# Kernel tuning notes

Measured on AMD Instinct MI355X. Metric: run time of the kernel, lower is better.

## Reference

```python
import jax, jax.numpy as jnp
import numpy as np


def setup_inputs() -> dict:
    key = jax.random.key(0)
    k1, k2 = jax.random.split(key)
    B, C, H, W = 8, 64, 32, 32
    K = 8192
    x = jax.random.normal(k1, (B, C, H, W), dtype=jnp.float32)
    codebook = jax.random.normal(k2, (K, C), dtype=jnp.float32)
    return {"x": x, "codebook": codebook}


def reference(x, codebook):
    """Faithful JAX version of VQVAE.quantize().

    x:        [B, C, H, W] latent (output of pre_quant_conv)
    codebook: [K, C] embedding weight
    Returns (quant_out [B,C,H,W], commitment_loss, codebook_loss, indices [B,H,W]).
    """
    B, C, H, W = x.shape
    # [B, H, W, C] -> [B, N, C]
    xf = jnp.transpose(x, (0, 2, 3, 1)).reshape(B, H * W, C)

    # Squared pairwise distances (argmin of cdist == argmin of squared dist).
    x2 = jnp.sum(xf * xf, axis=-1, keepdims=True)            # [B, N, 1]
    e2 = jnp.sum(codebook * codebook, axis=-1)               # [K]
    xe = jnp.einsum('bnc,kc->bnk', xf, codebook)             # [B, N, K]
    d2 = x2 + e2[None, None, :] - 2.0 * xe                   # [B, N, K]
    idx = jnp.argmin(d2, axis=-1)                            # [B, N]

    quant = codebook[idx.reshape(-1)]                        # [B*N, C]
    xflat = xf.reshape(-1, C)                                # [B*N, C]

    commitment_loss = jnp.mean((jax.lax.stop_gradient(quant) - xflat) ** 2)
    codebook_loss = jnp.mean((quant - jax.lax.stop_gradient(xflat)) ** 2)

    # Straight-through estimator.
    quant_st = xflat + jax.lax.stop_gradient(quant - xflat)
    quant_out = jnp.transpose(quant_st.reshape(B, H, W, C), (0, 3, 1, 2))
    indices = idx.reshape(B, H, W)
    return quant_out, commitment_loss, codebook_loss, indices
```

## Files before the change

### kernel.cpp

```cpp
#include <hip/hip_runtime.h>


#define N_PTS   8192
#define K_CODES 8192
#define C_DIM   64
#define HWSZ    1024
#define QOUT_N  524288
#define SPLITS  16

#define WS_XS    0
#define WS_CBS   2097152
#define WS_E2H   4194304
#define WS_PACK  4227072
#define WS_PART  5275648

typedef __attribute__((ext_vector_type(8))) short    short8;
typedef __attribute__((ext_vector_type(8))) _Float16 half8;
typedef __attribute__((ext_vector_type(4))) float    floatx4;

__device__ __forceinline__ half8 as_h8(short8 v) {
    return __builtin_bit_cast(half8, v);
}
__device__ __forceinline__ void split2(float v, unsigned short& h,
                                       unsigned short& m) {
    _Float16 hh = (_Float16)v;
    float r = v - (float)hh;
    _Float16 mm = (_Float16)r;
    h = __builtin_bit_cast(unsigned short, hh);
    m = __builtin_bit_cast(unsigned short, mm);
}
__device__ __forceinline__ void cp16(const void* g, void* l) {
    __builtin_amdgcn_global_load_lds(
        (const __attribute__((address_space(1))) void*)g,
        (__attribute__((address_space(3))) void*)l, 16, 0, 0);
}
__device__ __forceinline__ void cp4(const void* g, void* l) {
    __builtin_amdgcn_global_load_lds(
        (const __attribute__((address_space(1))) void*)g,
        (__attribute__((address_space(3))) void*)l, 4, 0, 0);
}

__global__ __launch_bounds__(256)
void vq_prep_kernel(const float* __restrict__ x,
                    const float* __restrict__ cb,
                    unsigned short* __restrict__ xS,
                    unsigned short* __restrict__ cbS,
                    float* __restrict__ e2h)
{
    const int bx  = blockIdx.x;
    const int tid = threadIdx.x;

    if (bx < 32) {
        const int k = bx * 256 + tid;
        const float* row = cb + k * C_DIM;
        float s = 0.0f;
        #pragma unroll
        for (int g = 0; g < 8; ++g) {
            float4 a = *(const float4*)(row + g * 8);
            float4 b = *(const float4*)(row + g * 8 + 4);
            float vv[8] = {a.x, a.y, a.z, a.w, b.x, b.y, b.z, b.w};
            unsigned short h8[8], m8[8];
            #pragma unroll
            for (int j = 0; j < 8; ++j) {
                s = fmaf(vv[j], vv[j], s);
                split2(vv[j], h8[j], m8[j]);
            }
            *(uint4*)(cbS + ((size_t)(0 * 8 + g) * 8192 + k) * 8) = *(const uint4*)h8;
            *(uint4*)(cbS + ((size_t)(1 * 8 + g) * 8192 + k) * 8) = *(const uint4*)m8;
        }
        e2h[k] = 0.5f * s;
    } else {
        const int u = bx - 32;
        const int b = u >> 5, g = (u >> 2) & 7, q = u & 3;
        const int hw = q * 256 + tid;
        const float* xb = x + (size_t)(b * C_DIM + g * 8) * HWSZ + hw;
        unsigned short h8[8], m8[8];
        #pragma unroll
        for (int cq = 0; cq < 8; ++cq)
            split2(xb[cq * HWSZ], h8[cq], m8[cq]);
        const size_t n = (size_t)b * 1024 + hw;
        *(uint4*)(xS + ((size_t)(0 * 8 + g) * 8192 + n) * 8) = *(const uint4*)h8;
        *(uint4*)(xS + ((size_t)(1 * 8 + g) * 8192 + n) * 8) = *(const uint4*)m8;
    }
}

#define SEG_SHORTS 512
#define NSEGS      16
#define BUF_SHORTS 8320

__device__ __forceinline__ void computeTile(const half8 af[4][2][2],
                                            const unsigned short* __restrict__ bsrc,
                                            int tl, int quad, int col, int code,
                                            float bestv[4][4], int besti[4][4])
{
    half8 bf[2][2];
    #pragma unroll
    for (int p = 0; p < 2; ++p)
        #pragma unroll
        for (int s = 0; s < 2; ++s) {
            int seg = p * 8 + s * 4 + quad;
            bf[p][s] = as_h8(*(const short8*)(bsrc + seg * SEG_SHORTS + (tl * 16 + col) * 8));
        }
    float me2 = -((const float*)(bsrc + NSEGS * SEG_SHORTS))[tl * 16 + col];

    floatx4 acc[4];
    #pragma unroll
    for (int t = 0; t < 4; ++t) acc[t] = (floatx4){me2, me2, me2, me2};

    #pragma unroll
    for (int s = 0; s < 2; ++s) {
        #pragma unroll
        for (int t = 0; t < 4; ++t)
            acc[t] = __builtin_amdgcn_mfma_f32_16x16x32_f16(af[t][0][s], bf[0][s], acc[t], 0, 0, 0);
        #pragma unroll
        for (int t = 0; t < 4; ++t)
            acc[t] = __builtin_amdgcn_mfma_f32_16x16x32_f16(af[t][0][s], bf[1][s], acc[t], 0, 0, 0);
        #pragma unroll
        for (int t = 0; t < 4; ++t)
            acc[t] = __builtin_amdgcn_mfma_f32_16x16x32_f16(af[t][1][s], bf[0][s], acc[t], 0, 0, 0);
    }

    #pragma unroll
    for (int t = 0; t < 4; ++t)
        #pragma unroll
        for (int r = 0; r < 4; ++r) {
            float sc = acc[t][r];
            bool gt = sc > bestv[t][r];
            bestv[t][r] = gt ? sc   : bestv[t][r];
            besti[t][r] = gt ? code : besti[t][r];
        }
}

__global__ __launch_bounds__(512, 1)
void vq_argmin_kernel(const unsigned short* __restrict__ xS,
                      const unsigned short* __restrict__ cbS,
                      const float* __restrict__ e2h,
                      unsigned long long* __restrict__ packedS)
{
    __shared__ __align__(16) unsigned short sBuf[2][BUF_SHORTS];

    const int tid   = threadIdx.x;
    const int lane  = tid & 63;
    const int w     = tid >> 6;
    const int col   = lane & 15;
    const int quad  = lane >> 4;
    const int mb    = blockIdx.x;
    const int split = blockIdx.y;
    const int m0    = mb * 512 + w * 64;
    const int nb0   = split * 512;

    half8 af[4][2][2];
    #pragma unroll
    for (int t = 0; t < 4; ++t) {
        int pt = m0 + t * 16 + col;
        #pragma unroll
        for (int p = 0; p < 2; ++p)
            #pragma unroll
            for (int s = 0; s < 2; ++s) {
                int g = s * 4 + quad;
                af[t][p][s] = as_h8(*(const short8*)(xS + ((size_t)(p * 8 + g) * 8192 + pt) * 8));
            }
    }

    float bestv[4][4];
    int   besti[4][4];
    #pragma unroll
    for (int t = 0; t < 4; ++t)
        #pragma unroll
        for (int r = 0; r < 4; ++r) {
            bestv[t][r] = __uint_as_float(0xFF800000u);
            besti[t][r] = 0;
        }

    auto stage = [&](int k0, int buf) {
        unsigned short* dst = &sBuf[buf][0];
        #pragma unroll
        for (int i = 0; i < 2; ++i) {
            int f   = tid + i * 512;
            int seg = f >> 6;
            int l   = f & 63;
            cp16(cbS + ((size_t)seg * 8192 + k0 + l) * 8,
                 dst + seg * SEG_SHORTS + l * 8);
        }
        if (tid < 64)
            cp4(e2h + k0 + tid, (float*)(dst + NSEGS * SEG_SHORTS) + tid);
    };

    stage(nb0, 0);
    __syncthreads();

    for (int ch = 0; ch < 8; ++ch) {
        if (ch + 1 < 8) stage(nb0 + (ch + 1) * 64, (ch + 1) & 1);
        const unsigned short* bsrc = &sBuf[ch & 1][0];
        #pragma unroll
        for (int tl = 0; tl < 4; ++tl)
            computeTile(af, bsrc, tl, quad, col,
                        nb0 + ch * 64 + tl * 16 + col, bestv, besti);
        __syncthreads();
    }

    unsigned long long own = 0;
    #pragma unroll
    for (int t = 0; t < 4; ++t)
        #pragma unroll
        for (int r = 0; r < 4; ++r) {
            unsigned u = __float_as_uint(-bestv[t][r]);
            u = ((int)u < 0) ? ~u : (u | 0x80000000u);
            unsigned long long p = ((unsigned long long)u << 32) | (unsigned)besti[t][r];
            #pragma unroll
            for (int msk = 1; msk < 16; msk <<= 1) {
                unsigned long long q = __shfl_xor(p, msk, 64);
                p = (q < p) ? q : p;
            }
            own = (col == t * 4 + r) ? p : own;
        }
    const int mpt = m0 + (col >> 2) * 16 + quad * 4 + (col & 3);
    packedS[(size_t)split * N_PTS + mpt] = own;
}

__global__ __launch_bounds__(256)
void vq_gather_kernel(const float* __restrict__ x,
                      const float* __restrict__ cb,
                      const unsigned long long* __restrict__ packedS,
                      float* __restrict__ out,
                      float* __restrict__ part)
{
    __shared__ unsigned long long sred[8][32];
    const int tid = threadIdx.x;
    const int p   = tid & 31;
    const int sg  = tid >> 5;
    const int n0  = blockIdx.x * 32;
    const int n   = n0 + p;

    {
        unsigned long long v = packedS[(size_t)(sg * 2) * N_PTS + n];
        unsigned long long q = packedS[(size_t)(sg * 2 + 1) * N_PTS + n];
        sred[sg][p] = (q < v) ? q : v;
    }
    __syncthreads();

    unsigned long long v = sred[0][p];
    #pragma unroll
    for (int s = 1; s < 8; ++s) {
        unsigned long long q = sred[s][p];
        v = (q < v) ? q : v;
    }
    const int idx = (int)(v & 0xFFFFFFFFull);
    if (tid < 32) out[QOUT_N + 2 + n0 + tid] = (float)idx;

    const int c0  = sg * 8;
    const int b   = n >> 10;
    const int hw  = n & 1023;
    const float* xb = x   + (size_t)b * (C_DIM * HWSZ) + hw;
    float*       ob = out + (size_t)b * (C_DIM * HWSZ) + hw;

    float s = 0.0f;
    #pragma unroll
    for (int c4 = 0; c4 < 2; ++c4) {
        float4 q = *(const float4*)(cb + (size_t)idx * C_DIM + c0 + c4 * 4);
        float qa[4] = {q.x, q.y, q.z, q.w};
        #pragma unroll
        for (int j = 0; j < 4; ++j) {
            int c = c0 + c4 * 4 + j;
            float xv = xb[c * HWSZ];
            float d  = qa[j] - xv;
            s = fmaf(d, d, s);
            ob[c * HWSZ] = xv + d;
        }
    }

    #pragma unroll
    for (int off = 32; off > 0; off >>= 1) s += __shfl_down(s, off, 64);
    if ((tid & 63) == 0) part[blockIdx.x * 4 + (tid >> 6)] = s;
}

__global__ __launch_bounds__(256)
void vq_final_kernel(const float* __restrict__ part, float* __restrict__ out)
{
    __shared__ float w[4];
    float s = part[threadIdx.x] + part[threadIdx.x + 256]
            + part[threadIdx.x + 512] + part[threadIdx.x + 768];
    #pragma unroll
    for (int off = 32; off > 0; off >>= 1) s += __shfl_down(s, off, 64);
    if ((threadIdx.x & 63) == 0) w[threadIdx.x >> 6] = s;
    __syncthreads();
    if (threadIdx.x == 0) {
        float m = (w[0] + w[1] + w[2] + w[3]) * (1.0f / (float)QOUT_N);
        out[QOUT_N]     = m;
        out[QOUT_N + 1] = m;
    }
}

extern "C" void kernel_launch(void* const* d_in, const int* in_sizes, int n_in,
                              void* d_out, int out_size, void* d_ws, size_t ws_size,
                              hipStream_t stream)
{
    const float* x  = (const float*)d_in[0];
    const float* cb = (const float*)d_in[1];
    float* out = (float*)d_out;
    char*  ws  = (char*)d_ws;
    (void)ws_size;

    unsigned short* xS  = (unsigned short*)(ws + WS_XS);
    unsigned short* cbS = (unsigned short*)(ws + WS_CBS);
    float* e2h = (float*)(ws + WS_E2H);
    unsigned long long* packedS = (unsigned long long*)(ws + WS_PACK);
    float* part = (float*)(ws + WS_PART);

    vq_prep_kernel<<<288, 256, 0, stream>>>(x, cb, xS, cbS, e2h);
    vq_argmin_kernel<<<dim3(16, SPLITS), 512, 0, stream>>>(xS, cbS, e2h, packedS);
    vq_gather_kernel<<<256, 256, 0, stream>>>(x, cb, packedS, out, part);
    vq_final_kernel<<<1, 256, 0, stream>>>(part, out);
}
```

Baseline: 90.31 us.

## Double argmin LDS chunk size and fold final loss reduction into gather via atomics

The argmin kernel now stages 128 codes per chunk instead of 64, which halves the number of chunk iterations and block barriers but doubles the LDS buffer size. The final one-block reduction kernel is removed: the gather kernel adds each wavefront's scaled partial loss to the output with atomicAdd, and the prep kernel zeroes the two loss slots first. This saves one kernel launch, but the float summation order becomes nondeterministic and the larger LDS footprint may lower occupancy.

```diff
diff --git a/kernel.cpp b/kernel.cpp
--- a/kernel.cpp
+++ b/kernel.cpp
@@ -12,7 +12,6 @@
 #define WS_CBS   2097152
 #define WS_E2H   4194304
 #define WS_PACK  4227072
-#define WS_PART  5275648
 
 typedef __attribute__((ext_vector_type(8))) short    short8;
 typedef __attribute__((ext_vector_type(8))) _Float16 half8;
@@ -45,10 +44,16 @@
                     const float* __restrict__ cb,
                     unsigned short* __restrict__ xS,
                     unsigned short* __restrict__ cbS,
-                    float* __restrict__ e2h)
+                    float* __restrict__ e2h,
+                    float* __restrict__ out)
 {
     const int bx  = blockIdx.x;
     const int tid = threadIdx.x;
+
+    if (bx == 0 && tid == 0) {
+        out[QOUT_N]     = 0.0f;
+        out[QOUT_N + 1] = 0.0f;
+    }
 
     if (bx < 32) {
         const int k = bx * 256 + tid;
@@ -84,13 +89,13 @@
     }
 }
 
-#define SEG_SHORTS 512
+#define SEG_SHORTS 1024
 #define NSEGS      16
-#define BUF_SHORTS 8320
+#define BUF_SHORTS 16640
 
 __device__ __forceinline__ void computeTile(const half8 af[4][2][2],
                                             const unsigned short* __restrict__ bsrc,
-                                            int tl, int quad, int col, int code,
+                                            int lc, int quad, int code,
                                             float bestv[4][4], int besti[4][4])
 {
     half8 bf[2][2];
@@ -99,9 +104,9 @@
         #pragma unroll
         for (int s = 0; s < 2; ++s) {
             int seg = p * 8 + s * 4 + quad;
-            bf[p][s] = as_h8(*(const short8*)(bsrc + seg * SEG_SHORTS + (tl * 16 + col) * 8));
-        }
-    float me2 = -((const float*)(bsrc + NSEGS * SEG_SHORTS))[tl * 16 + col];
+            bf[p][s] = as_h8(*(const short8*)(bsrc + seg * SEG_SHORTS + lc * 8));
+        }
+    float me2 = -((const float*)(bsrc + NSEGS * SEG_SHORTS))[lc];
 
     floatx4 acc[4];
     #pragma unroll
@@ -175,27 +180,32 @@
     auto stage = [&](int k0, int buf) {
         unsigned short* dst = &sBuf[buf][0];
         #pragma unroll
-        for (int i = 0; i < 2; ++i) {
+        for (int i = 0; i < 4; ++i) {
             int f   = tid + i * 512;
-            int seg = f >> 6;
-            int l   = f & 63;
+            int seg = f >> 7;
+            int l   = f & 127;
             cp16(cbS + ((size_t)seg * 8192 + k0 + l) * 8,
                  dst + seg * SEG_SHORTS + l * 8);
         }
-        if (tid < 64)
+        if (tid < 128)
             cp4(e2h + k0 + tid, (float*)(dst + NSEGS * SEG_SHORTS) + tid);
     };
 
     stage(nb0, 0);
     __syncthreads();
 
-    for (int ch = 0; ch < 8; ++ch) {
-        if (ch + 1 < 8) stage(nb0 + (ch + 1) * 64, (ch + 1) & 1);
+    for (int ch = 0; ch < 4; ++ch) {
+        if (ch + 1 < 4) stage(nb0 + (ch + 1) * 128, (ch + 1) & 1);
         const unsigned short* bsrc = &sBuf[ch & 1][0];
-        #pragma unroll
-        for (int tl = 0; tl < 4; ++tl)
-            computeTile(af, bsrc, tl, quad, col,
-                        nb0 + ch * 64 + tl * 16 + col, bestv, besti);
+        #pragma unroll 1
+        for (int grp = 0; grp < 2; ++grp) {
+            #pragma unroll
+            for (int tl = 0; tl < 4; ++tl) {
+                int lc = grp * 64 + tl * 16 + col;
+                computeTile(af, bsrc, lc, quad,
+                            nb0 + ch * 128 + lc, bestv, besti);
+            }
+        }
         __syncthreads();
     }
 
@@ -222,8 +232,7 @@
 void vq_gather_kernel(const float* __restrict__ x,
                       const float* __restrict__ cb,
                       const unsigned long long* __restrict__ packedS,
-                      float* __restrict__ out,
-                      float* __restrict__ part)
+                      float* __restrict__ out)
 {
     __shared__ unsigned long long sred[8][32];
     const int tid = threadIdx.x;
@@ -271,23 +280,10 @@
 
     #pragma unroll
     for (int off = 32; off > 0; off >>= 1) s += __shfl_down(s, off, 64);
-    if ((tid & 63) == 0) part[blockIdx.x * 4 + (tid >> 6)] = s;
-}
-
-__global__ __launch_bounds__(256)
-void vq_final_kernel(const float* __restrict__ part, float* __restrict__ out)
-{
-    __shared__ float w[4];
-    float s = part[threadIdx.x] + part[threadIdx.x + 256]
-            + part[threadIdx.x + 512] + part[threadIdx.x + 768];
-    #pragma unroll
-    for (int off = 32; off > 0; off >>= 1) s += __shfl_down(s, off, 64);
-    if ((threadIdx.x & 63) == 0) w[threadIdx.x >> 6] = s;
-    __syncthreads();
-    if (threadIdx.x == 0) {
-        float m = (w[0] + w[1] + w[2] + w[3]) * (1.0f / (float)QOUT_N);
-        out[QOUT_N]     = m;
-        out[QOUT_N + 1] = m;
+    if ((tid & 63) == 0) {
+        float m = s * (1.0f / (float)QOUT_N);
+        atomicAdd(out + QOUT_N,     m);
+        atomicAdd(out + QOUT_N + 1, m);
     }
 }
 
@@ -305,10 +301,8 @@
     unsigned short* cbS = (unsigned short*)(ws + WS_CBS);
     float* e2h = (float*)(ws + WS_E2H);
     unsigned long long* packedS = (unsigned long long*)(ws + WS_PACK);
-    float* part = (float*)(ws + WS_PART);
-
-    vq_prep_kernel<<<288, 256, 0, stream>>>(x, cb, xS, cbS, e2h);
+
+    vq_prep_kernel<<<288, 256, 0, stream>>>(x, cb, xS, cbS, e2h, out);
     vq_argmin_kernel<<<dim3(16, SPLITS), 512, 0, stream>>>(xS, cbS, e2h, packedS);
-    vq_gather_kernel<<<256, 256, 0, stream>>>(x, cb, packedS, out, part);
-    vq_final_kernel<<<1, 256, 0, stream>>>(part, out);
-}
+    vq_gather_kernel<<<256, 256, 0, stream>>>(x, cb, packedS, out);
+}
```

Measured after the change: 114.0 us. +26.2%, slower.
